# Performance work log

Measured on AMD Instinct MI355X. Metric: run time of the kernel, lower is better.

## Reference

```python
import jax, jax.numpy as jnp
import numpy as np
import math

N, FB, D, H, HD, L, K = 512, 256, 64, 128, 4, 4, 100
# note: H=num_heads=4, HD=head_dim=128 -> inner dim H*HD = 512
H, HD = 4, 128
HHD = H * HD
EPS = 1e-5


def mish(x):
    return x * jnp.tanh(jax.nn.softplus(x))


def layer_norm(x, g, b):
    mu = jnp.mean(x, axis=-1, keepdims=True)
    var = jnp.var(x, axis=-1, keepdims=True)
    return (x - mu) * jax.lax.rsqrt(var + EPS) * g + b


def setup_inputs() -> dict:
    key = jax.random.key(0)
    ks = jax.random.split(key, 16)
    def lin(k, fan_in, shape):
        return jax.random.normal(k, shape, jnp.float32) / np.sqrt(fan_in)
    return {
        "node_features": jax.random.normal(ks[0], (N, FB), jnp.float32),
        "amds": jax.random.uniform(ks[1], (N, K), jnp.float32),
        "emb_W": lin(ks[2], FB, (FB, D)),
        "emb_b": jnp.zeros((D,), jnp.float32),
        "bias_emb_W": lin(ks[3], K, (K, D)),
        "bias_emb_b": jnp.zeros((D,), jnp.float32),
        "ln1_g": jnp.ones((D,), jnp.float32),
        "ln1_b": jnp.zeros((D,), jnp.float32),
        "ln2_g": jnp.ones((D,), jnp.float32),
        "ln2_b": jnp.zeros((D,), jnp.float32),
        "qkv_W": lin(ks[4], D, (L, D, 3 * HHD)),
        "qkv_b": jnp.zeros((L, 3 * HHD), jnp.float32),
        "diff_W": lin(ks[5], D, (L, D, HHD)),
        "diff_b": jnp.zeros((L, HHD), jnp.float32),
        "o_W": lin(ks[6], HHD, (L, HHD, D)),
        "o_b": jnp.zeros((L, D), jnp.float32),
        "bout_W": lin(ks[7], HHD, (L, HHD, D)),
        "bout_b": jnp.zeros((L, D), jnp.float32),
        "out_W": lin(ks[8], D, (D, 1)),
        "out_b": jnp.zeros((1,), jnp.float32),
    }


def reference(node_features, amds, emb_W, emb_b, bias_emb_W, bias_emb_b,
              ln1_g, ln1_b, ln2_g, ln2_b, qkv_W, qkv_b, diff_W, diff_b,
              o_W, o_b, bout_W, bout_b, out_W, out_b):
    h = node_features @ emb_W + emb_b                     # [N, D]
    b0 = amds @ bias_emb_W + bias_emb_b                   # [N, D]
    bias = b0[None, :, :] - b0[:, None, :]                # [N, N, D]
    x = layer_norm(h, ln1_g, ln1_b)
    scale = 1.0 / math.sqrt(HD)
    for l in range(L):
        qkv = (x @ qkv_W[l] + qkv_b[l]).reshape(N, H, 3 * HD)
        q, k, v = jnp.split(qkv, 3, axis=-1)              # each [N, H, HD]
        be = mish(bias @ diff_W[l] + diff_b[l])           # [N, N, H*HD]
        diffs = jnp.linalg.norm(be.reshape(N, N, H, HD), axis=-1)  # [N, N, H]
        diffs = jnp.transpose(diffs, (2, 0, 1))           # [H, N, N]
        logits = jnp.einsum('nhd,mhd->hnm', q, k) * scale + diffs
        attn = jax.nn.softmax(logits, axis=-1)            # [H, N, N]
        vals = jnp.einsum('hnm,mhd->nhd', attn, v).reshape(N, HHD)
        temp_x = vals @ o_W[l] + o_b[l]                   # [N, D]
        bias = mish(be @ bout_W[l] + bout_b[l])           # [N, N, D]
        x = layer_norm(x + temp_x, ln2_g, ln2_b)
    return x @ out_W + out_b                              # [N, 1]
```

## Files before the change

### kernel.cpp

```cpp
#include <hip/hip_runtime.h>
#include <hip/hip_bf16.h>
#include <hip/hip_fp16.h>
#include <cmath>


namespace {

constexpr int kN   = 512;
constexpr int kD   = 64;
constexpr int kH   = 4;
constexpr int kHD  = 128;
constexpr int kHHD = 512;
constexpr int kFB  = 256;
constexpr int kK   = 100;
constexpr float kEps   = 1e-5f;
constexpr float kScale = 0.08838834764831845f;

typedef unsigned short u16;
typedef unsigned int u32;
typedef short bf16x8 __attribute__((ext_vector_type(8)));
typedef _Float16 f16x8 __attribute__((ext_vector_type(8)));
typedef float f32x4 __attribute__((ext_vector_type(4)));

__device__ __forceinline__ float mish_f(float x) {
    float e  = __expf(x);
    float n2 = fmaf(e, e + 2.0f, 2.0f);
    return fmaf(x + x, -__builtin_amdgcn_rcpf(n2), x);
}

__device__ __forceinline__ u32 pkh(float a, float b) {
    union { __half2 h; u32 u; } cv;
    cv.h = __float22half2_rn(make_float2(a, b));
    return cv.u;
}
__device__ __forceinline__ f16x8 mkh8(u32 a, u32 b, u32 c, u32 d) {
    union { u32 w[4]; f16x8 v; } cv;
    cv.w[0] = a; cv.w[1] = b; cv.w[2] = c; cv.w[3] = d;
    return cv.v;
}
__device__ __forceinline__ u16 f16_bits(float f) {
    union { __half h; u16 u; } cv;
    cv.h = __float2half(f);
    return cv.u;
}

__device__ __forceinline__ void ld4(float* d, const float* s) {
    float4 v = *(const float4*)s;
    d[0] = v.x; d[1] = v.y; d[2] = v.z; d[3] = v.w;
}

__global__ __launch_bounds__(64) void embed_kernel(
    const float* __restrict__ nf, const float* __restrict__ amds,
    const float* __restrict__ emb_W, const float* __restrict__ emb_b,
    const float* __restrict__ bemb_W, const float* __restrict__ bemb_b,
    const float* __restrict__ ln1_g, const float* __restrict__ ln1_b,
    float* __restrict__ x, float* __restrict__ b0)
{
    const int n = blockIdx.x;
    const int d = threadIdx.x;
    __shared__ float s_row[kFB];
    #pragma unroll
    for (int r = 0; r < kFB / kD; ++r) s_row[r * kD + d] = nf[n * kFB + r * kD + d];
    __syncthreads();
    float acc = emb_b[d];
    for (int k = 0; k < kFB; ++k) acc = fmaf(s_row[k], emb_W[k * kD + d], acc);
    float mu = acc;
    #pragma unroll
    for (int off = 32; off > 0; off >>= 1) mu += __shfl_xor(mu, off);
    mu *= (1.0f / kD);
    float dv = acc - mu;
    float var = dv * dv;
    #pragma unroll
    for (int off = 32; off > 0; off >>= 1) var += __shfl_xor(var, off);
    var *= (1.0f / kD);
    x[n * kD + d] = dv * rsqrtf(var + kEps) * ln1_g[d] + ln1_b[d];
    __syncthreads();
    s_row[d] = amds[n * kK + d];
    if (d < kK - kD) s_row[kD + d] = amds[n * kK + kD + d];
    __syncthreads();
    float bacc = bemb_b[d];
    for (int k = 0; k < kK; ++k) bacc = fmaf(s_row[k], bemb_W[k * kD + d], bacc);
    b0[n * kD + d] = bacc;
}

__global__ __launch_bounds__(256) void bias_init_kernel(
    const float* __restrict__ b0, u16* __restrict__ bias)
{
    int gid = blockIdx.x * 256 + threadIdx.x;
    int d8 = gid & 7;
    int j  = (gid >> 3) & (kN - 1);
    int i  = gid >> 12;
    const float4* bj = (const float4*)(b0 + j * kD + d8 * 8);
    const float4* bi = (const float4*)(b0 + i * kD + d8 * 8);
    float4 a0 = bj[0], a1 = bj[1];
    float4 c0 = bi[0], c1 = bi[1];
    union { u32 w[4]; bf16x8 v; } cv;
    cv.w[0] = pkh(a0.x - c0.x, a0.y - c0.y);
    cv.w[1] = pkh(a0.z - c0.z, a0.w - c0.w);
    cv.w[2] = pkh(a1.x - c1.x, a1.y - c1.y);
    cv.w[3] = pkh(a1.z - c1.z, a1.w - c1.w);
    *(bf16x8*)(bias + (long)gid * 8) = cv.v;
}

__global__ __launch_bounds__(256) void prep_weights_kernel(
    const float* __restrict__ diff_W, const float* __restrict__ bout_W,
    u16* __restrict__ dWt, u16* __restrict__ boutWt)
{
    int gid = blockIdx.x * 256 + threadIdx.x;
    if (gid < 4 * 32768) {
        int e = gid;
        int l = e >> 15;
        int r = e & 32767;
        int k = r >> 9;
        int n = r & 511;
        dWt[l * 32768 + n * 64 + k] = f16_bits(diff_W[e]);
    } else {
        int e = gid - 4 * 32768;
        int l = e >> 15;
        int r = e & 32767;
        int k = r >> 6;
        int d = r & 63;
        boutWt[l * 32768 + d * 512 + k] = f16_bits(bout_W[e]);
    }
}

__global__ __launch_bounds__(256) void qkv_kernel(
    const float* __restrict__ x, const float* __restrict__ W,
    const float* __restrict__ b, float* __restrict__ qkv)
{
    const int n = blockIdx.y;
    const int c = blockIdx.x * 256 + threadIdx.x;
    __shared__ float s_x[kD];
    if (threadIdx.x < kD) s_x[threadIdx.x] = x[n * kD + threadIdx.x];
    __syncthreads();
    float acc = b[c];
    #pragma unroll 8
    for (int d = 0; d < kD; ++d) acc = fmaf(s_x[d], W[d * (3 * kHHD) + c], acc);
    qkv[n * (3 * kHHD) + c] = acc;
}

__global__ __launch_bounds__(256, 4) void bias_layer_mfma(
    u16* __restrict__ bias,
    const u16* __restrict__ dWt, const u16* __restrict__ boutWt,
    const float* __restrict__ diff_b, const float* __restrict__ bout_b,
    float* __restrict__ diffs, int last)
{
    __shared__ u16 s_w[2][4096];
    __shared__ float s_db[kHHD];

    const int t    = threadIdx.x;
    const int w    = t >> 6;
    const int lane = t & 63;
    const int q    = lane >> 4;
    const int c    = lane & 15;
    const int pb   = blockIdx.x * 128 + w * 32;

    const int sb_bc  = t >> 3;
    const int sb_kb  = t & 7;
    const int sr     = ((sb_bc >> 2) & 1) * 16 + ((sb_bc >> 3) << 2) + (sb_bc & 3);
    const int w1_dst = sr * 64 + (sb_kb ^ (sr & 7)) * 8;
    const int sb_d   = t >> 2;
    const int sb_k2  = t & 3;
    const int w2_dst = 2048 + sb_d * 32 + (sb_k2 ^ ((sb_d >> 1) & 3)) * 8;
    const u16* g_w1 = dWt + sb_bc * 64 + sb_kb * 8;
    const u16* g_w2 = boutWt + sb_d * 512 + sb_k2 * 8;

    f16x8 Bf[2][2];
    #pragma unroll
    for (int mt = 0; mt < 2; ++mt) {
        #pragma unroll
        for (int s = 0; s < 2; ++s) {
            Bf[mt][s] = *(const f16x8*)(bias + (long)(pb + mt * 16 + c) * kD + s * 32 + q * 8);
        }
    }

    {
        bf16x8 r0 = *(const bf16x8*)g_w1;
        bf16x8 r1 = *(const bf16x8*)g_w2;
        *(bf16x8*)&s_w[0][w1_dst] = r0;
        *(bf16x8*)&s_w[0][w2_dst] = r1;
        s_db[t] = diff_b[t];
        s_db[256 + t] = diff_b[256 + t];
    }
    __syncthreads();

    f32x4 acc2[2][4];
    #pragma unroll
    for (int mt = 0; mt < 2; ++mt)
        #pragma unroll
        for (int dg = 0; dg < 4; ++dg) acc2[mt][dg] = (f32x4)0.0f;
    float psum[2][4];
    #pragma unroll
    for (int mt = 0; mt < 2; ++mt)
        #pragma unroll
        for (int h = 0; h < 4; ++h) psum[mt][h] = 0.0f;

    const int sw1 = c & 7;
    const int sw2 = (c >> 1) & 3;
    int cur = 0;

    for (int g2 = 0; g2 < 16; ++g2) {
        bf16x8 r0, r1;
        if (g2 < 15) {
            r0 = *(const bf16x8*)(g_w1 + (g2 + 1) * 2048);
            r1 = *(const bf16x8*)(g_w2 + (g2 + 1) * 32);
        }

        f32x4 a1[2][2];
        #pragma unroll
        for (int mt = 0; mt < 2; ++mt)
            #pragma unroll
            for (int u = 0; u < 2; ++u) a1[mt][u] = (f32x4)0.0f;
        const u16* w1 = &s_w[cur][0];
        #pragma unroll
        for (int u = 0; u < 2; ++u) {
            int row = (u * 16 + c) * 64;
            int o0 = row + ((0 + q) ^ sw1) * 8;
            int o1 = row + ((4 + q) ^ sw1) * 8;
            f16x8 A0 = *(const f16x8*)(w1 + o0);
            f16x8 A1 = *(const f16x8*)(w1 + o1);
            #pragma unroll
            for (int mt = 0; mt < 2; ++mt) {
                a1[mt][u] = __builtin_amdgcn_mfma_f32_16x16x32_f16(A0, Bf[mt][0], a1[mt][u], 0, 0, 0);
                a1[mt][u] = __builtin_amdgcn_mfma_f32_16x16x32_f16(A1, Bf[mt][1], a1[mt][u], 0, 0, 0);
            }
        }

        const int hd = g2 >> 2;
        const float4 db0 = *(const float4*)&s_db[g2 * 32 + q * 8];
        const float4 db1 = *(const float4*)&s_db[g2 * 32 + q * 8 + 4];
        f16x8 A2[2];
        #pragma unroll
        for (int mt = 0; mt < 2; ++mt) {
            u32 p[2][2];
            #pragma unroll
            for (int u = 0; u < 2; ++u) {
                const float4 db = u ? db1 : db0;
                float v0 = mish_f(a1[mt][u][0] + db.x);
                float v1 = mish_f(a1[mt][u][1] + db.y);
                float v2 = mish_f(a1[mt][u][2] + db.z);
                float v3 = mish_f(a1[mt][u][3] + db.w);
                psum[mt][hd] += v0 * v0 + v1 * v1 + v2 * v2 + v3 * v3;
                p[u][0] = pkh(v0, v1);
                p[u][1] = pkh(v2, v3);
            }
            A2[mt] = mkh8(p[0][0], p[0][1], p[1][0], p[1][1]);
        }

        if (!last) {
            const u16* w2 = &s_w[cur][2048];
            const int kb2 = (q ^ sw2) * 8;
            #pragma unroll
            for (int dg = 0; dg < 4; ++dg) {
                int bo = dg * 512 + c * 32 + kb2;
                f16x8 Wf = *(const f16x8*)(w2 + bo);
                #pragma unroll
                for (int mt = 0; mt < 2; ++mt) {
                    acc2[mt][dg] = __builtin_amdgcn_mfma_f32_16x16x32_f16(A2[mt], Wf, acc2[mt][dg], 0, 0, 0);
                }
            }
        }

        if (g2 < 15) {
            int nb = cur ^ 1;
            *(bf16x8*)&s_w[nb][w1_dst] = r0;
            *(bf16x8*)&s_w[nb][w2_dst] = r1;
            __syncthreads();
            cur = nb;
        }
    }

    if (!last) {
        #pragma unroll
        for (int mt = 0; mt < 2; ++mt) {
            #pragma unroll
            for (int dg = 0; dg < 4; ++dg) {
                float bb = bout_b[dg * 16 + c];
                #pragma unroll
                for (int r = 0; r < 4; ++r) {
                    float v = mish_f(acc2[mt][dg][r] + bb);
                    bias[(long)(pb + mt * 16 + 4 * q + r) * kD + dg * 16 + c] = f16_bits(v);
                }
            }
        }
    }
    const int i  = blockIdx.x >> 2;
    const int jb = (blockIdx.x & 3) * 128 + w * 32;
    #pragma unroll
    for (int mt = 0; mt < 2; ++mt) {
        #pragma unroll
        for (int h = 0; h < 4; ++h) {
            psum[mt][h] += __shfl_xor(psum[mt][h], 16);
            psum[mt][h] += __shfl_xor(psum[mt][h], 32);
        }
        float sv = (q == 0) ? psum[mt][0] : (q == 1) ? psum[mt][1]
                 : (q == 2) ? psum[mt][2] : psum[mt][3];
        diffs[q * (kN * kN) + i * kN + jb + mt * 16 + c] = sqrtf(sv);
    }
}

__global__ __launch_bounds__(256) void logits_kernel(
    const float* __restrict__ qkv, const float* __restrict__ diffs,
    float* __restrict__ logits)
{
    constexpr int SW = 68;
    __shared__ float s_q[32 * SW];
    __shared__ float s_k[64 * SW];
    const int t  = threadIdx.x;
    const int tX = t & 15;
    const int tY = t >> 4;
    const int h  = blockIdx.z;
    const int n0 = blockIdx.x * 32;
    const int m0 = blockIdx.y * 64;

    float acc[2][4];
    #pragma unroll
    for (int a = 0; a < 2; ++a)
        #pragma unroll
        for (int b = 0; b < 4; ++b) acc[a][b] = 0.0f;

    for (int dc = 0; dc < 2; ++dc) {
        __syncthreads();
        #pragma unroll
        for (int rep = 0; rep < 2; ++rep) {
            int f = rep * 256 + t;
            int row = f >> 4;
            int c4  = f & 15;
            *(float4*)&s_q[row * SW + c4 * 4] =
                *(const float4*)&qkv[(n0 + row) * (3 * kHHD) + h * 384 + dc * 64 + c4 * 4];
        }
        #pragma unroll
        for (int rep = 0; rep < 4; ++rep) {
            int f = rep * 256 + t;
            int row = f >> 4;
            int c4  = f & 15;
            *(float4*)&s_k[row * SW + c4 * 4] =
                *(const float4*)&qkv[(m0 + row) * (3 * kHHD) + h * 384 + 128 + dc * 64 + c4 * 4];
        }
        __syncthreads();
        for (int d = 0; d < 64; d += 4) {
            float a[2][4], b[4][4];
            #pragma unroll
            for (int rr = 0; rr < 2; ++rr) ld4(a[rr], &s_q[(tY + 16 * rr) * SW + d]);
            #pragma unroll
            for (int cc = 0; cc < 4; ++cc) ld4(b[cc], &s_k[(tX + 16 * cc) * SW + d]);
            #pragma unroll
            for (int rr = 0; rr < 2; ++rr)
                #pragma unroll
                for (int cc = 0; cc < 4; ++cc)
                    #pragma unroll
                    for (int u = 0; u < 4; ++u)
                        acc[rr][cc] = fmaf(a[rr][u], b[cc][u], acc[rr][cc]);
        }
    }
    #pragma unroll
    for (int rr = 0; rr < 2; ++rr)
        #pragma unroll
        for (int cc = 0; cc < 4; ++cc) {
            int row = n0 + tY + 16 * rr;
            int col = m0 + tX + 16 * cc;
            long idx = (long)h * (kN * kN) + (long)row * kN + col;
            logits[idx] = acc[rr][cc] * kScale + diffs[idx];
        }
}

__global__ __launch_bounds__(256) void softmax_kernel(float* __restrict__ logits)
{
    const int row = blockIdx.x;
    float* p = logits + (long)row * kN;
    const int t = threadIdx.x;
    float v0 = p[t];
    float v1 = p[t + 256];
    float m = fmaxf(v0, v1);
    #pragma unroll
    for (int off = 32; off > 0; off >>= 1) m = fmaxf(m, __shfl_xor(m, off));
    __shared__ float s_red[4];
    __shared__ float s_sum[4];
    if ((t & 63) == 0) s_red[t >> 6] = m;
    __syncthreads();
    m = fmaxf(fmaxf(s_red[0], s_red[1]), fmaxf(s_red[2], s_red[3]));
    float e0 = expf(v0 - m);
    float e1 = expf(v1 - m);
    float s = e0 + e1;
    #pragma unroll
    for (int off = 32; off > 0; off >>= 1) s += __shfl_xor(s, off);
    if ((t & 63) == 0) s_sum[t >> 6] = s;
    __syncthreads();
    s = (s_sum[0] + s_sum[1]) + (s_sum[2] + s_sum[3]);
    float inv = 1.0f / s;
    p[t] = e0 * inv;
    p[t + 256] = e1 * inv;
}

__global__ __launch_bounds__(256) void attnv_kernel(
    const float* __restrict__ attn, const float* __restrict__ qkv,
    float* __restrict__ vpart)
{
    constexpr int SW = 68;
    __shared__ float s_p[32 * SW];
    __shared__ float s_v[64 * SW];
    const int t  = threadIdx.x;
    const int tx = t & 15;
    const int ty = t >> 4;
    const int h  = blockIdx.z & 3;
    const int mq = blockIdx.z >> 2;
    const int n0 = blockIdx.x * 32;
    const int d0 = blockIdx.y * 64;
    float* vp = vpart + (long)mq * (kN * kHHD);

    float acc[2][4];
    #pragma unroll
    for (int a = 0; a < 2; ++a)
        #pragma unroll
        for (int b = 0; b < 4; ++b) acc[a][b] = 0.0f;

    for (int mt = mq * 2; mt < mq * 2 + 2; ++mt) {
        const int m0 = mt * 64;
        __syncthreads();
        #pragma unroll
        for (int rep = 0; rep < 2; ++rep) {
            int f = rep * 256 + t;
            int row = f >> 4;
            int c4  = f & 15;
            *(float4*)&s_p[row * SW + c4 * 4] =
                *(const float4*)&attn[(long)h * (kN * kN) + (long)(n0 + row) * kN + m0 + c4 * 4];
        }
        #pragma unroll
        for (int rep = 0; rep < 4; ++rep) {
            int f = rep * 256 + t;
            int row = f >> 4;
            int c4  = f & 15;
            *(float4*)&s_v[row * SW + c4 * 4] =
                *(const float4*)&qkv[(m0 + row) * (3 * kHHD) + h * 384 + 256 + d0 + c4 * 4];
        }
        __syncthreads();
        for (int kk = 0; kk < 64; kk += 4) {
            float a[2][4], b[4][4];
            #pragma unroll
            for (int rr = 0; rr < 2; ++rr) ld4(a[rr], &s_p[(ty + 16 * rr) * SW + kk]);
            #pragma unroll
            for (int u = 0; u < 4; ++u) ld4(b[u], &s_v[(kk + u) * SW + 4 * tx]);
            #pragma unroll
            for (int rr = 0; rr < 2; ++rr)
                #pragma unroll
                for (int cc = 0; cc < 4; ++cc)
                    #pragma unroll
                    for (int u = 0; u < 4; ++u)
                        acc[rr][cc] = fmaf(a[rr][u], b[u][cc], acc[rr][cc]);
        }
    }
    #pragma unroll
    for (int rr = 0; rr < 2; ++rr) {
        float4 o = make_float4(acc[rr][0], acc[rr][1], acc[rr][2], acc[rr][3]);
        *(float4*)&vp[(long)(n0 + ty + 16 * rr) * kHHD + h * kHD + d0 + 4 * tx] = o;
    }
}

__global__ __launch_bounds__(256) void oproj_ln_kernel(
    const float* __restrict__ vpart, const float* __restrict__ o_W,
    const float* __restrict__ o_b, const float* __restrict__ g2,
    const float* __restrict__ b2, float* __restrict__ x)
{
    const int n = blockIdx.x;
    const int t = threadIdx.x;
    const int w = t >> 6;
    const int d = t & 63;
    __shared__ float s_v[kHHD];
    __shared__ float s_part[4][kD];
    #pragma unroll
    for (int r = 0; r < 2; ++r) {
        int j = r * 256 + t;
        s_v[j] = (vpart[n * kHHD + j] + vpart[kN * kHHD + n * kHHD + j])
               + (vpart[2 * (kN * kHHD) + n * kHHD + j] + vpart[3 * (kN * kHHD) + n * kHHD + j]);
    }
    __syncthreads();
    float acc = 0.0f;
    #pragma unroll 4
    for (int j = 0; j < 128; ++j)
        acc = fmaf(s_v[w * 128 + j], o_W[(w * 128 + j) * kD + d], acc);
    s_part[w][d] = acc;
    __syncthreads();
    if (t < kD) {
        float av = o_b[d] + ((s_part[0][d] + s_part[1][d]) + (s_part[2][d] + s_part[3][d]));
        float xv = x[n * kD + d] + av;
        float mu = xv;
        #pragma unroll
        for (int off = 32; off > 0; off >>= 1) mu += __shfl_xor(mu, off);
        mu *= (1.0f / kD);
        float dv = xv - mu;
        float var = dv * dv;
        #pragma unroll
        for (int off = 32; off > 0; off >>= 1) var += __shfl_xor(var, off);
        var *= (1.0f / kD);
        x[n * kD + d] = dv * rsqrtf(var + kEps) * g2[d] + b2[d];
    }
}

__global__ __launch_bounds__(64) void final_kernel(
    const float* __restrict__ x, const float* __restrict__ out_W,
    const float* __restrict__ out_b, float* __restrict__ out)
{
    const int n = blockIdx.x * 64 + threadIdx.x;
    float acc = out_b[0];
    #pragma unroll
    for (int d = 0; d < kD; ++d) acc = fmaf(x[n * kD + d], out_W[d], acc);
    out[n] = acc;
}

}

extern "C" void kernel_launch(void* const* d_in, const int* in_sizes, int n_in,
                              void* d_out, int out_size, void* d_ws, size_t ws_size,
                              hipStream_t stream)
{
    (void)in_sizes; (void)n_in; (void)out_size; (void)ws_size;

    const float* nf     = (const float*)d_in[0];
    const float* amds   = (const float*)d_in[1];
    const float* emb_W  = (const float*)d_in[2];
    const float* emb_b  = (const float*)d_in[3];
    const float* bemb_W = (const float*)d_in[4];
    const float* bemb_b = (const float*)d_in[5];
    const float* ln1_g  = (const float*)d_in[6];
    const float* ln1_b  = (const float*)d_in[7];
    const float* ln2_g  = (const float*)d_in[8];
    const float* ln2_b  = (const float*)d_in[9];
    const float* qkv_W  = (const float*)d_in[10];
    const float* qkv_b  = (const float*)d_in[11];
    const float* diff_W = (const float*)d_in[12];
    const float* diff_b = (const float*)d_in[13];
    const float* o_W    = (const float*)d_in[14];
    const float* o_b    = (const float*)d_in[15];
    const float* bout_W = (const float*)d_in[16];
    const float* bout_b = (const float*)d_in[17];
    const float* out_W  = (const float*)d_in[18];
    const float* out_b  = (const float*)d_in[19];

    float* ws = (float*)d_ws;
    float* ws_x      = ws;
    float* ws_b0     = ws_x + 32768;
    float* ws_qkv    = ws_b0 + 32768;
    float* ws_vals   = ws_qkv + 786432;
    float* ws_diffs  = ws_vals + 262144;
    float* ws_logits = ws_diffs + 1048576;
    u16*   ws_bias   = (u16*)(ws_logits + 1048576);
    u16*   dWt       = ws_bias + 16777216;
    u16*   boutWt    = dWt + 131072;

    embed_kernel<<<kN, kD, 0, stream>>>(nf, amds, emb_W, emb_b, bemb_W, bemb_b,
                                        ln1_g, ln1_b, ws_x, ws_b0);
    bias_init_kernel<<<(kN * kN * kD / 8) / 256, 256, 0, stream>>>(ws_b0, ws_bias);
    prep_weights_kernel<<<(2 * 4 * 32768) / 256, 256, 0, stream>>>(
        diff_W, bout_W, dWt, boutWt);

    for (int l = 0; l < 4; ++l) {
        qkv_kernel<<<dim3(6, kN), 256, 0, stream>>>(
            ws_x, qkv_W + l * kD * (3 * kHHD), qkv_b + l * (3 * kHHD), ws_qkv);
        bias_layer_mfma<<<kN * kN / 128, 256, 0, stream>>>(
            ws_bias, dWt + l * 32768, boutWt + l * 32768,
            diff_b + l * kHHD, bout_b + l * kD, ws_diffs, (l == 3) ? 1 : 0);
        logits_kernel<<<dim3(16, 8, kH), 256, 0, stream>>>(ws_qkv, ws_diffs, ws_logits);
        softmax_kernel<<<kH * kN, 256, 0, stream>>>(ws_logits);
        attnv_kernel<<<dim3(16, 2, 4 * kH), 256, 0, stream>>>(ws_logits, ws_qkv, ws_diffs);
        oproj_ln_kernel<<<kN, 256, 0, stream>>>(
            ws_diffs, o_W + l * kHHD * kD, o_b + l * kD, ln2_g, ln2_b, ws_x);
    }
    final_kernel<<<kN / kD, kD, 0, stream>>>(ws_x, out_W, out_b, (float*)d_out);
}
```

Before: 556.2 us.

## Fuse logits, softmax and attn-V into split-KV flash attention kernel

Replaces the separate logits, softmax and attention-times-V kernels with one kernel. It computes QK^T plus the diffs bias for a 16-row by 128-key tile, does a local softmax, and multiplies by V. Per-split max and sum are written out and merged in the o-projection/layernorm kernel. This removes the round trips of the full logits matrix through global memory and two kernel launches. The QKV projection also now computes 8 rows per block so each weight load is reused across rows.

```diff
diff --git a/kernel.cpp b/kernel.cpp
--- a/kernel.cpp
+++ b/kernel.cpp
@@ -42,11 +42,6 @@
     union { __half h; u16 u; } cv;
     cv.h = __float2half(f);
     return cv.u;
-}
-
-__device__ __forceinline__ void ld4(float* d, const float* s) {
-    float4 v = *(const float4*)s;
-    d[0] = v.x; d[1] = v.y; d[2] = v.z; d[3] = v.w;
 }
 
 __global__ __launch_bounds__(64) void embed_kernel(
@@ -128,15 +123,24 @@
     const float* __restrict__ x, const float* __restrict__ W,
     const float* __restrict__ b, float* __restrict__ qkv)
 {
-    const int n = blockIdx.y;
-    const int c = blockIdx.x * 256 + threadIdx.x;
-    __shared__ float s_x[kD];
-    if (threadIdx.x < kD) s_x[threadIdx.x] = x[n * kD + threadIdx.x];
-    __syncthreads();
-    float acc = b[c];
-    #pragma unroll 8
-    for (int d = 0; d < kD; ++d) acc = fmaf(s_x[d], W[d * (3 * kHHD) + c], acc);
-    qkv[n * (3 * kHHD) + c] = acc;
+    const int t  = threadIdx.x;
+    const int c  = blockIdx.x * 256 + t;
+    const int n0 = blockIdx.y * 8;
+    __shared__ float s_x[8 * kD];
+    s_x[t]       = x[n0 * kD + t];
+    s_x[256 + t] = x[n0 * kD + 256 + t];
+    __syncthreads();
+    float acc[8];
+    float bb = b[c];
+    #pragma unroll
+    for (int r = 0; r < 8; ++r) acc[r] = bb;
+    for (int d = 0; d < kD; ++d) {
+        float wv = W[d * (3 * kHHD) + c];
+        #pragma unroll
+        for (int r = 0; r < 8; ++r) acc[r] = fmaf(s_x[r * kD + d], wv, acc[r]);
+    }
+    #pragma unroll
+    for (int r = 0; r < 8; ++r) qkv[(n0 + r) * (3 * kHHD) + c] = acc[r];
 }
 
 __global__ __launch_bounds__(256, 4) void bias_layer_mfma(
@@ -299,167 +303,118 @@
     }
 }
 
-__global__ __launch_bounds__(256) void logits_kernel(
+__global__ __launch_bounds__(256) void flash_attn_kernel(
     const float* __restrict__ qkv, const float* __restrict__ diffs,
-    float* __restrict__ logits)
-{
-    constexpr int SW = 68;
-    __shared__ float s_q[32 * SW];
-    __shared__ float s_k[64 * SW];
-    const int t  = threadIdx.x;
-    const int tX = t & 15;
-    const int tY = t >> 4;
-    const int h  = blockIdx.z;
-    const int n0 = blockIdx.x * 32;
-    const int m0 = blockIdx.y * 64;
-
-    float acc[2][4];
-    #pragma unroll
-    for (int a = 0; a < 2; ++a)
-        #pragma unroll
-        for (int b = 0; b < 4; ++b) acc[a][b] = 0.0f;
-
-    for (int dc = 0; dc < 2; ++dc) {
-        __syncthreads();
-        #pragma unroll
-        for (int rep = 0; rep < 2; ++rep) {
-            int f = rep * 256 + t;
-            int row = f >> 4;
-            int c4  = f & 15;
-            *(float4*)&s_q[row * SW + c4 * 4] =
-                *(const float4*)&qkv[(n0 + row) * (3 * kHHD) + h * 384 + dc * 64 + c4 * 4];
-        }
-        #pragma unroll
-        for (int rep = 0; rep < 4; ++rep) {
-            int f = rep * 256 + t;
-            int row = f >> 4;
-            int c4  = f & 15;
-            *(float4*)&s_k[row * SW + c4 * 4] =
-                *(const float4*)&qkv[(m0 + row) * (3 * kHHD) + h * 384 + 128 + dc * 64 + c4 * 4];
-        }
-        __syncthreads();
-        for (int d = 0; d < 64; d += 4) {
-            float a[2][4], b[4][4];
-            #pragma unroll
-            for (int rr = 0; rr < 2; ++rr) ld4(a[rr], &s_q[(tY + 16 * rr) * SW + d]);
-            #pragma unroll
-            for (int cc = 0; cc < 4; ++cc) ld4(b[cc], &s_k[(tX + 16 * cc) * SW + d]);
-            #pragma unroll
-            for (int rr = 0; rr < 2; ++rr)
-                #pragma unroll
-                for (int cc = 0; cc < 4; ++cc)
-                    #pragma unroll
-                    for (int u = 0; u < 4; ++u)
-                        acc[rr][cc] = fmaf(a[rr][u], b[cc][u], acc[rr][cc]);
-        }
-    }
-    #pragma unroll
-    for (int rr = 0; rr < 2; ++rr)
-        #pragma unroll
-        for (int cc = 0; cc < 4; ++cc) {
-            int row = n0 + tY + 16 * rr;
-            int col = m0 + tX + 16 * cc;
-            long idx = (long)h * (kN * kN) + (long)row * kN + col;
-            logits[idx] = acc[rr][cc] * kScale + diffs[idx];
-        }
-}
-
-__global__ __launch_bounds__(256) void softmax_kernel(float* __restrict__ logits)
-{
-    const int row = blockIdx.x;
-    float* p = logits + (long)row * kN;
-    const int t = threadIdx.x;
-    float v0 = p[t];
-    float v1 = p[t + 256];
-    float m = fmaxf(v0, v1);
-    #pragma unroll
-    for (int off = 32; off > 0; off >>= 1) m = fmaxf(m, __shfl_xor(m, off));
-    __shared__ float s_red[4];
-    __shared__ float s_sum[4];
-    if ((t & 63) == 0) s_red[t >> 6] = m;
-    __syncthreads();
-    m = fmaxf(fmaxf(s_red[0], s_red[1]), fmaxf(s_red[2], s_red[3]));
-    float e0 = expf(v0 - m);
-    float e1 = expf(v1 - m);
-    float s = e0 + e1;
-    #pragma unroll
-    for (int off = 32; off > 0; off >>= 1) s += __shfl_xor(s, off);
-    if ((t & 63) == 0) s_sum[t >> 6] = s;
-    __syncthreads();
-    s = (s_sum[0] + s_sum[1]) + (s_sum[2] + s_sum[3]);
-    float inv = 1.0f / s;
-    p[t] = e0 * inv;
-    p[t + 256] = e1 * inv;
-}
-
-__global__ __launch_bounds__(256) void attnv_kernel(
-    const float* __restrict__ attn, const float* __restrict__ qkv,
-    float* __restrict__ vpart)
-{
-    constexpr int SW = 68;
-    __shared__ float s_p[32 * SW];
-    __shared__ float s_v[64 * SW];
+    float* __restrict__ part, float* __restrict__ ml)
+{
+    __shared__ float s_a[16 * 132];
+    __shared__ float s_b[128 * 36];
+
     const int t  = threadIdx.x;
     const int tx = t & 15;
     const int ty = t >> 4;
-    const int h  = blockIdx.z & 3;
-    const int mq = blockIdx.z >> 2;
-    const int n0 = blockIdx.x * 32;
-    const int d0 = blockIdx.y * 64;
-    float* vp = vpart + (long)mq * (kN * kHHD);
-
-    float acc[2][4];
-    #pragma unroll
-    for (int a = 0; a < 2; ++a)
-        #pragma unroll
-        for (int b = 0; b < 4; ++b) acc[a][b] = 0.0f;
-
-    for (int mt = mq * 2; mt < mq * 2 + 2; ++mt) {
-        const int m0 = mt * 64;
+    const int n0 = blockIdx.x * 16;
+    const int mq = blockIdx.y;
+    const int h  = blockIdx.z;
+    const int m0 = mq * 128;
+
+    #pragma unroll
+    for (int rep = 0; rep < 2; ++rep) {
+        int f = rep * 256 + t;
+        int row = f >> 5;
+        int c4  = f & 31;
+        *(float4*)&s_a[row * 132 + c4 * 4] =
+            *(const float4*)&qkv[(n0 + row) * (3 * kHHD) + h * 384 + c4 * 4];
+    }
+
+    float acc[8];
+    #pragma unroll
+    for (int cc = 0; cc < 8; ++cc) acc[cc] = 0.0f;
+
+    for (int db = 0; db < 4; ++db) {
         __syncthreads();
-        #pragma unroll
-        for (int rep = 0; rep < 2; ++rep) {
-            int f = rep * 256 + t;
-            int row = f >> 4;
-            int c4  = f & 15;
-            *(float4*)&s_p[row * SW + c4 * 4] =
-                *(const float4*)&attn[(long)h * (kN * kN) + (long)(n0 + row) * kN + m0 + c4 * 4];
-        }
         #pragma unroll
         for (int rep = 0; rep < 4; ++rep) {
             int f = rep * 256 + t;
-            int row = f >> 4;
-            int c4  = f & 15;
-            *(float4*)&s_v[row * SW + c4 * 4] =
-                *(const float4*)&qkv[(m0 + row) * (3 * kHHD) + h * 384 + 256 + d0 + c4 * 4];
+            int row = f >> 3;
+            int c4  = f & 7;
+            *(float4*)&s_b[row * 36 + c4 * 4] =
+                *(const float4*)&qkv[(m0 + row) * (3 * kHHD) + h * 384 + 128 + db * 32 + c4 * 4];
         }
         __syncthreads();
-        for (int kk = 0; kk < 64; kk += 4) {
-            float a[2][4], b[4][4];
-            #pragma unroll
-            for (int rr = 0; rr < 2; ++rr) ld4(a[rr], &s_p[(ty + 16 * rr) * SW + kk]);
-            #pragma unroll
-            for (int u = 0; u < 4; ++u) ld4(b[u], &s_v[(kk + u) * SW + 4 * tx]);
-            #pragma unroll
-            for (int rr = 0; rr < 2; ++rr)
-                #pragma unroll
-                for (int cc = 0; cc < 4; ++cc)
-                    #pragma unroll
-                    for (int u = 0; u < 4; ++u)
-                        acc[rr][cc] = fmaf(a[rr][u], b[u][cc], acc[rr][cc]);
-        }
-    }
-    #pragma unroll
-    for (int rr = 0; rr < 2; ++rr) {
-        float4 o = make_float4(acc[rr][0], acc[rr][1], acc[rr][2], acc[rr][3]);
-        *(float4*)&vp[(long)(n0 + ty + 16 * rr) * kHHD + h * kHD + d0 + 4 * tx] = o;
+        #pragma unroll 2
+        for (int k4 = 0; k4 < 8; ++k4) {
+            float4 a = *(const float4*)&s_a[ty * 132 + db * 32 + k4 * 4];
+            #pragma unroll
+            for (int cc = 0; cc < 8; ++cc) {
+                float4 b = *(const float4*)&s_b[(tx + 16 * cc) * 36 + k4 * 4];
+                acc[cc] = fmaf(a.x, b.x, acc[cc]);
+                acc[cc] = fmaf(a.y, b.y, acc[cc]);
+                acc[cc] = fmaf(a.z, b.z, acc[cc]);
+                acc[cc] = fmaf(a.w, b.w, acc[cc]);
+            }
+        }
+    }
+
+    #pragma unroll
+    for (int cc = 0; cc < 8; ++cc) {
+        acc[cc] = acc[cc] * kScale +
+                  diffs[h * (kN * kN) + (n0 + ty) * kN + m0 + tx + 16 * cc];
+    }
+    float mrow = acc[0];
+    #pragma unroll
+    for (int cc = 1; cc < 8; ++cc) mrow = fmaxf(mrow, acc[cc]);
+    #pragma unroll
+    for (int off = 1; off < 16; off <<= 1) mrow = fmaxf(mrow, __shfl_xor(mrow, off));
+    float lrow = 0.0f;
+    #pragma unroll
+    for (int cc = 0; cc < 8; ++cc) {
+        float p = __expf(acc[cc] - mrow);
+        acc[cc] = p;
+        lrow += p;
+    }
+    #pragma unroll
+    for (int off = 1; off < 16; off <<= 1) lrow += __shfl_xor(lrow, off);
+
+    __syncthreads();
+    #pragma unroll
+    for (int cc = 0; cc < 8; ++cc) s_a[ty * 132 + tx + 16 * cc] = acc[cc];
+    if (tx == 0) {
+        *(float2*)&ml[((h * 4 + mq) * kN + n0 + ty) * 2] = make_float2(mrow, lrow);
+    }
+
+    const int pbase = (h * 4 + mq) * (kN * kHD) + (n0 + ty) * kHD;
+    for (int db = 0; db < 4; ++db) {
+        __syncthreads();
+        #pragma unroll
+        for (int rep = 0; rep < 4; ++rep) {
+            int f = rep * 256 + t;
+            int row = f >> 3;
+            int c4  = f & 7;
+            *(float4*)&s_b[row * 36 + c4 * 4] =
+                *(const float4*)&qkv[(m0 + row) * (3 * kHHD) + h * 384 + 256 + db * 32 + c4 * 4];
+        }
+        __syncthreads();
+        float a0 = 0.0f, a1 = 0.0f;
+        for (int c4 = 0; c4 < 32; ++c4) {
+            float4 pa = *(const float4*)&s_a[ty * 132 + c4 * 4];
+            #pragma unroll
+            for (int u = 0; u < 4; ++u) {
+                float pu = (u == 0) ? pa.x : (u == 1) ? pa.y : (u == 2) ? pa.z : pa.w;
+                float2 vv = *(const float2*)&s_b[(c4 * 4 + u) * 36 + tx * 2];
+                a0 = fmaf(pu, vv.x, a0);
+                a1 = fmaf(pu, vv.y, a1);
+            }
+        }
+        *(float2*)&part[pbase + db * 32 + tx * 2] = make_float2(a0, a1);
     }
 }
 
 __global__ __launch_bounds__(256) void oproj_ln_kernel(
-    const float* __restrict__ vpart, const float* __restrict__ o_W,
-    const float* __restrict__ o_b, const float* __restrict__ g2,
-    const float* __restrict__ b2, float* __restrict__ x)
+    const float* __restrict__ part, const float* __restrict__ ml,
+    const float* __restrict__ o_W, const float* __restrict__ o_b,
+    const float* __restrict__ g2, const float* __restrict__ b2,
+    float* __restrict__ x)
 {
     const int n = blockIdx.x;
     const int t = threadIdx.x;
@@ -469,9 +424,28 @@
     __shared__ float s_part[4][kD];
     #pragma unroll
     for (int r = 0; r < 2; ++r) {
-        int j = r * 256 + t;
-        s_v[j] = (vpart[n * kHHD + j] + vpart[kN * kHHD + n * kHHD + j])
-               + (vpart[2 * (kN * kHHD) + n * kHHD + j] + vpart[3 * (kN * kHHD) + n * kHHD + j]);
+        int j  = r * 256 + t;
+        int h  = j >> 7;
+        int dd = j & 127;
+        float2 m_l[4];
+        float M = -1e30f;
+        #pragma unroll
+        for (int q = 0; q < 4; ++q) {
+            m_l[q] = *(const float2*)&ml[((h * 4 + q) * kN + n) * 2];
+            M = fmaxf(M, m_l[q].x);
+        }
+        float L = 0.0f, wq[4];
+        #pragma unroll
+        for (int q = 0; q < 4; ++q) {
+            wq[q] = __expf(m_l[q].x - M);
+            L = fmaf(wq[q], m_l[q].y, L);
+        }
+        float sv = 0.0f;
+        #pragma unroll
+        for (int q = 0; q < 4; ++q) {
+            sv = fmaf(wq[q], part[(h * 4 + q) * (kN * kHD) + n * kHD + dd], sv);
+        }
+        s_v[j] = sv / L;
     }
     __syncthreads();
     float acc = 0.0f;
@@ -540,10 +514,10 @@
     float* ws_x      = ws;
     float* ws_b0     = ws_x + 32768;
     float* ws_qkv    = ws_b0 + 32768;
-    float* ws_vals   = ws_qkv + 786432;
-    float* ws_diffs  = ws_vals + 262144;
-    float* ws_logits = ws_diffs + 1048576;
-    u16*   ws_bias   = (u16*)(ws_logits + 1048576);
+    float* ws_ml     = ws_qkv + 786432;
+    float* ws_diffs  = ws_ml + 262144;
+    float* ws_part   = ws_diffs + 1048576;
+    u16*   ws_bias   = (u16*)(ws_part + 1048576);
     u16*   dWt       = ws_bias + 16777216;
     u16*   boutWt    = dWt + 131072;
 
@@ -554,16 +528,15 @@
         diff_W, bout_W, dWt, boutWt);
 
     for (int l = 0; l < 4; ++l) {
-        qkv_kernel<<<dim3(6, kN), 256, 0, stream>>>(
+        qkv_kernel<<<dim3(6, 64), 256, 0, stream>>>(
             ws_x, qkv_W + l * kD * (3 * kHHD), qkv_b + l * (3 * kHHD), ws_qkv);
         bias_layer_mfma<<<kN * kN / 128, 256, 0, stream>>>(
             ws_bias, dWt + l * 32768, boutWt + l * 32768,
             diff_b + l * kHHD, bout_b + l * kD, ws_diffs, (l == 3) ? 1 : 0);
-        logits_kernel<<<dim3(16, 8, kH), 256, 0, stream>>>(ws_qkv, ws_diffs, ws_logits);
-        softmax_kernel<<<kH * kN, 256, 0, stream>>>(ws_logits);
-        attnv_kernel<<<dim3(16, 2, 4 * kH), 256, 0, stream>>>(ws_logits, ws_qkv, ws_diffs);
+        flash_attn_kernel<<<dim3(32, 4, kH), 256, 0, stream>>>(
+            ws_qkv, ws_diffs, ws_part, ws_ml);
         oproj_ln_kernel<<<kN, 256, 0, stream>>>(
-            ws_diffs, o_W + l * kHHD * kD, o_b + l * kD, ln2_g, ln2_b, ws_x);
+            ws_part, ws_ml, o_W + l * kHHD * kD, o_b + l * kD, ln2_g, ln2_b, ws_x);
     }
     final_kernel<<<kN / kD, kD, 0, stream>>>(ws_x, out_W, out_b, (float*)d_out);
 }
```

After: 541.9 us. 2.6% less time.
